# Kernel tuning notes

Measured on AMD Instinct MI355X. Metric: run time of the kernel, lower is better.

Reference implementation:

```python
import jax, jax.numpy as jnp
import numpy as np

NEG_SLOPE_GAT = 0.2   # PyG GATConv default negative_slope
NEG_SLOPE = 0.01      # torch.nn.LeakyReLU default
NUM_AISLES = 20       # aisle_nrs drawn from [0,20); matches aisle_nrs.max()+1


def leaky(x, s):
    return jnp.where(x >= 0, x, s * x)


def gat_conv(x, src, dst, W, a_src, a_dst, b, n_nodes):
    """Single-head PyG GATConv (self-loops already appended to src/dst)."""
    h = x @ W                                        # [N, C]
    es = h @ a_src                                   # [N]
    ed = h @ a_dst                                   # [N]
    e = leaky(es[src] + ed[dst], NEG_SLOPE_GAT)      # [E] per-edge score
    m = jax.ops.segment_max(e, dst, num_segments=n_nodes)
    w = jnp.exp(e - m[dst])
    z = jax.ops.segment_sum(w, dst, num_segments=n_nodes)
    alpha = w / z[dst]                               # segment softmax over incoming edges
    out = jax.ops.segment_sum(h[src] * alpha[:, None], dst, num_segments=n_nodes)
    return out + b


def setup_inputs() -> dict:
    key = jax.random.key(0)
    ks = jax.random.split(key, 32)
    B, N, E = 16, 2048, 32768
    Fin, H, O, HA = 32, 128, 64, 256

    def glorot(k, shape):
        fan = shape[0] + shape[-1]
        return jax.random.uniform(k, shape, jnp.float32, -1.0, 1.0) * np.sqrt(6.0 / fan)

    inp = {
        "graph_nodes": jax.random.normal(ks[0], (B, N, Fin), jnp.float32),
        "aisle_nrs": jax.random.randint(ks[1], (B, N), 0, NUM_AISLES),
        "graph_edge_links": jax.random.randint(ks[2], (B, 2, E), 0, N),
        "mask": jax.random.randint(ks[3], (B, N), 0, 2),
        "picks_left": jax.random.randint(ks[4], (B,), 0, 100),
        # GAT layer 1: Fin -> H
        "W1": glorot(ks[5], (Fin, H)), "as1": glorot(ks[6], (H,)), "ad1": glorot(ks[7], (H,)), "b1": jnp.zeros((H,), jnp.float32),
        # GAT layer 2: H -> H
        "W2": glorot(ks[8], (H, H)), "as2": glorot(ks[9], (H,)), "ad2": glorot(ks[10], (H,)), "b2": jnp.zeros((H,), jnp.float32),
        # GAT layer 3: H -> O
        "W3": glorot(ks[11], (H, O)), "as3": glorot(ks[12], (O,)), "ad3": glorot(ks[13], (O,)), "b3": jnp.zeros((O,), jnp.float32),
        # post-embedding MLP head
        "lw1": glorot(ks[14], (2 * O, HA)), "lb1": jnp.zeros((HA,), jnp.float32),
        "lw2": glorot(ks[15], (HA, O)), "lb2": jnp.zeros((O,), jnp.float32),
        "lw3": glorot(ks[16], (O, 1)), "lb3": jnp.zeros((1,), jnp.float32),
    }
    return inp


def reference(graph_nodes, aisle_nrs, graph_edge_links, mask, picks_left,
              W1, as1, ad1, b1, W2, as2, ad2, b2, W3, as3, ad3, b3,
              lw1, lb1, lw2, lb2, lw3, lb3):
    B, N, Fin = graph_nodes.shape
    NT = B * N
    x = graph_nodes.reshape(NT, Fin)

    # batch the graphs: offset per-graph edge indices, append self-loops
    off = (jnp.arange(B) * N)[:, None]
    src = (graph_edge_links[:, 0, :] + off).reshape(-1)
    dst = (graph_edge_links[:, 1, :] + off).reshape(-1)
    loops = jnp.arange(NT)
    src = jnp.concatenate([src, loops])
    dst = jnp.concatenate([dst, loops])

    x = gat_conv(x, src, dst, W1, as1, ad1, b1, NT)
    x = gat_conv(x, src, dst, W2, as2, ad2, b2, NT)
    x = gat_conv(x, src, dst, W3, as3, ad3, b3, NT)

    # scatter-mean aisle embedding
    batch_idx = jnp.repeat(jnp.arange(B), N)
    aid = aisle_nrs.reshape(-1) + batch_idx * NUM_AISLES   # [NT]
    S = B * NUM_AISLES
    ssum = jax.ops.segment_sum(x, aid, num_segments=S)
    cnt = jax.ops.segment_sum(jnp.ones((NT,), x.dtype), aid, num_segments=S)
    emb = ssum / jnp.maximum(cnt, 1.0)[:, None]

    x = jnp.concatenate([x, emb[aid]], axis=1)             # [NT, 2*O]
    x = leaky(x @ lw1 + lb1, NEG_SLOPE)
    x = leaky(x @ lw2 + lb2, NEG_SLOPE)
    x = (x @ lw3 + lb3).reshape(B, N)

    logits = jnp.where(mask != 0, x, -jnp.inf)
    return jax.nn.softmax(logits, axis=1)
```

## Files before the change

kernel.cpp:

```cpp
#include <hip/hip_runtime.h>
#include <hip/hip_bf16.h>
#include <math.h>
#include <stdint.h>

#define BATCH 16
#define NNODE 2048
#define EPG   32768
#define NT    (BATCH * NNODE)
#define ET    (BATCH * EPG + NT)
#define NUM_AISLES 20
#define SEG   (BATCH * NUM_AISLES)
#define NEG_GAT 0.2f
#define NEG_MLP 0.01f
#define ACHUNK 8
#define CAP 64
#define EMB_LD 72

typedef __attribute__((ext_vector_type(8))) short s16x8;
typedef __attribute__((ext_vector_type(4))) float f32x4;

__device__ __forceinline__ void split_bf16(float v, unsigned short& hi, unsigned short& lo) {
    unsigned int u = __float_as_uint(v);
    unsigned int r = u + 0x7FFFu + ((u >> 16) & 1u);
    hi = (unsigned short)(r >> 16);
    float fh = __uint_as_float(((unsigned int)hi) << 16);
    float rem = v - fh;
    unsigned int u2 = __float_as_uint(rem);
    unsigned int r2 = u2 + 0x7FFFu + ((u2 >> 16) & 1u);
    lo = (unsigned short)(r2 >> 16);
}

__device__ __forceinline__ unsigned int pack_bf16(float v) {
    unsigned short h, l;
    split_bf16(v, h, l);
    return ((unsigned int)h << 16) | l;
}

__device__ __forceinline__ float unpack_f32(unsigned int u) {
    return __uint_as_float(u & 0xffff0000u) + __uint_as_float(u << 16);
}

union SU { s16x8 v; unsigned short u[8]; };

__device__ __forceinline__ void unpack_pair(const uint4& u0, const uint4& u1, SU& ah, SU& al) {
    unsigned int uu[8] = {u0.x, u0.y, u0.z, u0.w, u1.x, u1.y, u1.z, u1.w};
#pragma unroll
    for (int j = 0; j < 8; ++j) {
        ah.u[j] = (unsigned short)(uu[j] >> 16);
        al.u[j] = (unsigned short)uu[j];
    }
}

__device__ __forceinline__ void split_pair(const float4& v0, const float4& v1, SU& ah, SU& al) {
    float a8[8] = {v0.x, v0.y, v0.z, v0.w, v1.x, v1.y, v1.z, v1.w};
#pragma unroll
    for (int j = 0; j < 8; ++j) split_bf16(a8[j], ah.u[j], al.u[j]);
}

__device__ __forceinline__ int swz_row0(int bx) {
    int xcd = bx & 7, i = bx >> 3;
    int graph = xcd * 2 + (i >> 5);
    return graph * NNODE + (i & 31) * 64;
}

template <int K, int KC, int NOUT, int COLS>
__device__ __forceinline__ void prep_one(const float* __restrict__ W,
                                         unsigned short* __restrict__ dst, int idx) {
    constexpr int SWM = (KC >= 64) ? 7 : 3;
    int k = idx / NOUT, col = idx - k * NOUT;
    int ch = k / KC, kl = k - ch * KC;
    int ct = col / COLS, n = col - ct * COLS;
    int tile = ct * (K / KC) + ch;
    unsigned short h, l;
    split_bf16(W[idx], h, l);
    size_t base = (size_t)tile * (2 * COLS * KC);
    int pos = n * KC + (kl ^ ((n & SWM) << 3));
    dst[base + pos] = h;
    dst[base + COLS * KC + pos] = l;
}

__global__ __launch_bounds__(256) void prep_weights(const float* __restrict__ W1,
                                                    const float* __restrict__ W2,
                                                    const float* __restrict__ W3,
                                                    const float* __restrict__ lw1,
                                                    const float* __restrict__ lw2,
                                                    unsigned short* __restrict__ P1,
                                                    unsigned short* __restrict__ P2,
                                                    unsigned short* __restrict__ P3,
                                                    unsigned short* __restrict__ P4,
                                                    unsigned short* __restrict__ P5,
                                                    int* __restrict__ cnt,
                                                    int* __restrict__ scount) {
    int b = blockIdx.x, t = threadIdx.x;
    if (b < 16)        prep_one<32, 32, 128, 128>(W1, P1, b * 256 + t);
    else if (b < 80)   prep_one<128, 64, 128, 128>(W2, P2, (b - 16) * 256 + t);
    else if (b < 112)  prep_one<128, 128, 64, 64>(W3, P3, (b - 80) * 256 + t);
    else if (b < 240)  prep_one<128, 64, 256, 128>(lw1, P4, (b - 112) * 256 + t);
    else if (b < 304)  prep_one<256, 128, 64, 64>(lw2, P5, (b - 240) * 256 + t);
    else if (b < 432)  cnt[(b - 304) * 256 + t] = 0;
    else if (t < BATCH) scount[t] = 0;
}

__device__ __forceinline__ void scatter_body(int b, const int* __restrict__ links,
                                             int* __restrict__ cnt,
                                             int* __restrict__ col_bkt) {
    int s, d;
    if (b < 2048) {
        int xcd = b & 7, idx = b >> 3;
        int g = xcd * 2 + (idx >> 7);
        int chunk = idx & 127;
        int i = chunk * 256 + threadIdx.x;
        const int* pb = links + (size_t)g * 2 * EPG;
        s = pb[i] + (g << 11);
        d = pb[EPG + i] + (g << 11);
    } else {
        int b2 = b - 2048;
        int xcd = b2 & 7, idx = b2 >> 3;
        int g = xcd * 2 + (idx >> 3);
        int chunk = idx & 7;
        s = d = g * NNODE + chunk * 256 + threadIdx.x;
    }
    int pos = atomicAdd(&cnt[d], 1);
    if (pos < CAP) col_bkt[d * CAP + pos] = s;
}

template <int K, int KC, int NOUT, int COLS, bool LEAKY, bool ATTN, bool FINAL,
          bool CONCAT, bool PACKEDA, bool PACKOUT>
__device__ __forceinline__ void gemm_body(int bx, int by,
                                          const void* __restrict__ Aptr,
                                          const unsigned short* __restrict__ WP,
                                          const float* __restrict__ bias,
                                          void* __restrict__ outp,
                                          const float* __restrict__ a_src,
                                          const float* __restrict__ a_dst,
                                          float* __restrict__ es,
                                          float* __restrict__ ed,
                                          const float* __restrict__ psum,
                                          const int* __restrict__ pcnt,
                                          const int* __restrict__ aisle,
                                          const float* __restrict__ lw3,
                                          const float* __restrict__ lb3,
                                          const int* __restrict__ mask,
                                          float* __restrict__ logits,
                                          int* __restrict__ scount,
                                          float* __restrict__ smout) {
    constexpr int C = COLS / 16;
    constexpr int SWM = (KC >= 64) ? 7 : 3;
    constexpr int TILE_US = COLS * KC;
    constexpr int TB2 = 2 * TILE_US * 2;
    constexpr int NCH = K / KC;
    constexpr int NKS = KC / 32;
    constexpr int NPRE = CONCAT ? 2 : (K / 32);
    static_assert(TB2 % 4096 == 0, "chunk must be a multiple of one 256-thread 16B sweep");

    __shared__ unsigned short WS[2 * TILE_US];
    __shared__ float emb_s[CONCAT ? NUM_AISLES * EMB_LD : 1];

    const int tid = threadIdx.x;
    const int wave = tid >> 6, lane = tid & 63;
    const int quad = lane >> 4, l15 = lane & 15;
    const int row0 = swz_row0(bx);
    const int m = row0 + wave * 16 + l15;

    uint4 apu[(CONCAT || PACKEDA) ? NPRE : 1][2];
    float4 apf[(CONCAT || PACKEDA) ? 1 : NPRE][2];
#pragma unroll
    for (int t = 0; t < NPRE; ++t) {
        const int off = t * 32 + quad * 8;
        if constexpr (CONCAT) {
            const unsigned int* ap = (const unsigned int*)Aptr + (size_t)m * 64 + off;
            apu[t][0] = ((const uint4*)ap)[0];
            apu[t][1] = ((const uint4*)ap)[1];
        } else if constexpr (PACKEDA) {
            const unsigned int* ap = (const unsigned int*)Aptr + (size_t)m * K + off;
            apu[t][0] = ((const uint4*)ap)[0];
            apu[t][1] = ((const uint4*)ap)[1];
        } else {
            const float* sp = (const float*)Aptr + (size_t)m * K + off;
            apf[t][0] = ((const float4*)sp)[0];
            apf[t][1] = ((const float4*)sp)[1];
        }
    }

    int am = 0;
    if constexpr (CONCAT) {
        int g = row0 >> 11;
        for (int i = tid; i < NUM_AISLES * 64; i += 256) {
            int a = i >> 6, f = i & 63;
            float s = 0.f;
            int c = 0;
#pragma unroll
            for (int ch = 0; ch < ACHUNK; ++ch) {
                s += psum[((size_t)(g * ACHUNK + ch) * NUM_AISLES + a) * 64 + f];
                c += pcnt[(g * ACHUNK + ch) * NUM_AISLES + a];
            }
            emb_s[a * EMB_LD + f] = s / fmaxf((float)c, 1.0f);
        }
        am = aisle[m];
    }

    f32x4 acc[C];
#pragma unroll
    for (int c = 0; c < C; ++c)
#pragma unroll
        for (int v = 0; v < 4; ++v) acc[c][v] = 0.f;

#pragma unroll
    for (int cidx = 0; cidx < NCH; ++cidx) {
        const char* gsrc = (const char*)WP + (size_t)(by * NCH + cidx) * TB2;
#pragma unroll
        for (int s = 0; s < TB2 / 4096; ++s) {
            __builtin_amdgcn_global_load_lds(
                (const __attribute__((address_space(1))) void*)(gsrc + s * 4096 + wave * 1024 + lane * 16),
                (__attribute__((address_space(3))) void*)&WS[(s * 4096 + wave * 1024) >> 1],
                16, 0, 0);
        }
        __syncthreads();

#pragma unroll
        for (int ks = 0; ks < NKS; ++ks) {
            const int t = cidx * NKS + ks;
            SU ah, al;
            if constexpr (CONCAT) {
                if (t < 2) {
                    unpack_pair(apu[t & 1][0], apu[t & 1][1], ah, al);
                } else {
                    const float* ep = &emb_s[am * EMB_LD + (t * 32 + quad * 8 - 64)];
                    split_pair(((const float4*)ep)[0], ((const float4*)ep)[1], ah, al);
                }
            } else if constexpr (PACKEDA) {
                unpack_pair(apu[t][0], apu[t][1], ah, al);
            } else {
                split_pair(apf[t][0], apf[t][1], ah, al);
            }

            const int kq = ks * 32 + quad * 8;
#pragma unroll
            for (int c = 0; c < C; ++c) {
                int n = c * 16 + l15;
                int pos = n * KC + (kq ^ ((n & SWM) << 3));
                s16x8 wh = *(const s16x8*)&WS[pos];
                s16x8 wl = *(const s16x8*)&WS[TILE_US + pos];
                acc[c] = __builtin_amdgcn_mfma_f32_16x16x32_bf16(ah.v, wh, acc[c], 0, 0, 0);
                acc[c] = __builtin_amdgcn_mfma_f32_16x16x32_bf16(ah.v, wl, acc[c], 0, 0, 0);
                acc[c] = __builtin_amdgcn_mfma_f32_16x16x32_bf16(al.v, wh, acc[c], 0, 0, 0);
            }
        }
        if (cidx + 1 < NCH) __syncthreads();
    }
    if constexpr (FINAL) {
        const int g = row0 >> 11;
#pragma unroll
        for (int reg = 0; reg < 4; ++reg) {
            float p = 0.f;
#pragma unroll
            for (int c = 0; c < C; ++c) {
                int colx = c * 16 + l15;
                float v = acc[c][reg] + bias[colx];
                v = v >= 0.f ? v : NEG_MLP * v;
                p += v * lw3[colx];
            }
#pragma unroll
            for (int mk = 1; mk < 16; mk <<= 1) p += __shfl_xor(p, mk, 64);
            if (l15 == 0) {
                int row = row0 + wave * 16 + quad * 4 + reg;
                float lg = p + lb3[0];
                logits[row] = (mask[row] != 0) ? lg : -INFINITY;
            }
        }
        __threadfence();
        __syncthreads();
        __shared__ int slast;
        if (tid == 0) slast = (atomicAdd(&scount[g], 1) == 31) ? 1 : 0;
        __syncthreads();
        if (slast) {
            __threadfence();
            const float* lr = logits + g * NNODE;
            float* op = smout + g * NNODE;
            __shared__ float sred[4], sredz[4];
            float mx = -INFINITY;
            for (int i = tid; i < NNODE; i += 256) mx = fmaxf(mx, lr[i]);
#pragma unroll
            for (int off = 32; off; off >>= 1) mx = fmaxf(mx, __shfl_xor(mx, off, 64));
            if (lane == 0) sred[wave] = mx;
            __syncthreads();
            mx = fmaxf(fmaxf(sred[0], sred[1]), fmaxf(sred[2], sred[3]));
            float z = 0.f;
            for (int i = tid; i < NNODE; i += 256) z += __expf(lr[i] - mx);
#pragma unroll
            for (int off = 32; off; off >>= 1) z += __shfl_xor(z, off, 64);
            if (lane == 0) sredz[wave] = z;
            __syncthreads();
            z = sredz[0] + sredz[1] + sredz[2] + sredz[3];
            float invz = 1.0f / z;
            for (int i = tid; i < NNODE; i += 256) {
                float v = lr[i];
                op[i] = (v == -INFINITY) ? 0.f : __expf(v - mx) * invz;
            }
        }
    } else {
#pragma unroll
        for (int c = 0; c < C; ++c) {
            int colx = by * COLS + c * 16 + l15;
            float bv = bias ? bias[colx] : 0.f;
#pragma unroll
            for (int reg = 0; reg < 4; ++reg) {
                int row = row0 + wave * 16 + quad * 4 + reg;
                float v = acc[c][reg] + bv;
                if (LEAKY) v = v >= 0.f ? v : NEG_MLP * v;
                if constexpr (PACKOUT) {
                    ((unsigned int*)outp)[(size_t)row * NOUT + colx] = pack_bf16(v);
                } else {
                    ((float*)outp)[(size_t)row * NOUT + colx] = v;
                }
            }
        }
        if constexpr (ATTN) {
#pragma unroll
            for (int reg = 0; reg < 4; ++reg) {
                float ps = 0.f, pd = 0.f;
#pragma unroll
                for (int c = 0; c < C; ++c) {
                    int colx = c * 16 + l15;
                    float v = acc[c][reg];
                    ps += v * a_src[colx];
                    pd += v * a_dst[colx];
                }
#pragma unroll
                for (int mk = 1; mk < 16; mk <<= 1) {
                    ps += __shfl_xor(ps, mk, 64);
                    pd += __shfl_xor(pd, mk, 64);
                }
                if (l15 == 0) {
                    int row = row0 + wave * 16 + quad * 4 + reg;
                    es[row] = ps;
                    ed[row] = pd;
                }
            }
        }
    }
}

template <int K, int KC, int NOUT, int COLS, bool LEAKY, bool ATTN, bool FINAL,
          bool CONCAT, bool PACKEDA, bool PACKOUT>
__global__ __launch_bounds__(256) void gemm_mfma(const void* __restrict__ A,
                                                 const unsigned short* __restrict__ WP,
                                                 const float* __restrict__ bias,
                                                 void* __restrict__ out,
                                                 const float* __restrict__ a_src,
                                                 const float* __restrict__ a_dst,
                                                 float* __restrict__ es,
                                                 float* __restrict__ ed,
                                                 const float* __restrict__ psum,
                                                 const int* __restrict__ pcnt,
                                                 const int* __restrict__ aisle,
                                                 const float* __restrict__ lw3,
                                                 const float* __restrict__ lb3,
                                                 const int* __restrict__ mask,
                                                 float* __restrict__ logits,
                                                 int* __restrict__ scount,
                                                 float* __restrict__ smout) {
    gemm_body<K, KC, NOUT, COLS, LEAKY, ATTN, FINAL, CONCAT, PACKEDA, PACKOUT>(
        blockIdx.x, blockIdx.y, A, WP, bias, out, a_src, a_dst, es, ed,
        psum, pcnt, aisle, lw3, lb3, mask, logits, scount, smout);
}

__global__ __launch_bounds__(256) void gemm1_scatter(const float* __restrict__ A,
                                                     const unsigned short* __restrict__ WP,
                                                     float* __restrict__ out,
                                                     const float* __restrict__ a_src,
                                                     const float* __restrict__ a_dst,
                                                     float* __restrict__ es,
                                                     float* __restrict__ ed,
                                                     const int* __restrict__ links,
                                                     int* __restrict__ cnt,
                                                     int* __restrict__ col_bkt) {
    if (blockIdx.x >= NT / 64) {
        scatter_body(blockIdx.x - NT / 64, links, cnt, col_bkt);
        return;
    }
    gemm_body<32, 32, 128, 128, false, true, false, false, false, false>(
        blockIdx.x, 0, A, WP, nullptr, out, a_src, a_dst, es, ed,
        nullptr, nullptr, nullptr, nullptr, nullptr, nullptr, nullptr, nullptr, nullptr);
}

template <int HD>
__global__ __launch_bounds__(256) void gat_aggregate(const float* __restrict__ h,
                                                     const float* __restrict__ es,
                                                     const float* __restrict__ ed,
                                                     const int* __restrict__ cnt,
                                                     const int* __restrict__ col_bkt,
                                                     const float* __restrict__ bias,
                                                     unsigned int* __restrict__ out) {
    int b = blockIdx.x;
    int xcd = b & 7, q = b >> 3;
    int graph = xcd * 2 + (q >> 9);
    int node = graph * NNODE + (q & 511) * 4 + (threadIdx.x >> 6);
    int lane = threadIdx.x & 63;
    int deg = cnt[node];
    deg = deg < CAP ? deg : CAP;
    float edv = ed[node];

    float e0 = -INFINITY;
    int c0v = 0;
    if (lane < deg) {
        c0v = col_bkt[node * CAP + lane];
        float e = es[c0v] + edv;
        e0 = e >= 0.f ? e : NEG_GAT * e;
    }
    float m = e0;
#pragma unroll
    for (int off = 32; off; off >>= 1) m = fmaxf(m, __shfl_xor(m, off, 64));
    float z = __expf(e0 - m);
#pragma unroll
    for (int off = 32; off; off >>= 1) z += __shfl_xor(z, off, 64);
    float w0 = __expf(e0 - m) / z;

    const int quad = lane >> 4, l15 = lane & 15;
    if (HD == 128) {
        float a0 = 0.f, a1 = 0.f, a2 = 0.f, a3 = 0.f;
        float a4 = 0.f, a5 = 0.f, a6 = 0.f, a7 = 0.f;
        for (int jj = 0; jj < deg; jj += 4) {
            int j2 = jj + quad;
            int s = __shfl(c0v, j2, 64);
            float w = __shfl(w0, j2, 64);
            const float* base = h + (size_t)s * 128 + l15 * 8;
            float4 v0 = *(const float4*)base;
            float4 v1 = *(const float4*)(base + 4);
            a0 += w * v0.x; a1 += w * v0.y; a2 += w * v0.z; a3 += w * v0.w;
            a4 += w * v1.x; a5 += w * v1.y; a6 += w * v1.z; a7 += w * v1.w;
        }
#pragma unroll
        for (int off = 16; off <= 32; off <<= 1) {
            a0 += __shfl_xor(a0, off, 64); a1 += __shfl_xor(a1, off, 64);
            a2 += __shfl_xor(a2, off, 64); a3 += __shfl_xor(a3, off, 64);
            a4 += __shfl_xor(a4, off, 64); a5 += __shfl_xor(a5, off, 64);
            a6 += __shfl_xor(a6, off, 64); a7 += __shfl_xor(a7, off, 64);
        }
        if (quad == 0) {
            const float* bb = bias + l15 * 8;
            uint4 p0, p1;
            p0.x = pack_bf16(a0 + bb[0]); p0.y = pack_bf16(a1 + bb[1]);
            p0.z = pack_bf16(a2 + bb[2]); p0.w = pack_bf16(a3 + bb[3]);
            p1.x = pack_bf16(a4 + bb[4]); p1.y = pack_bf16(a5 + bb[5]);
            p1.z = pack_bf16(a6 + bb[6]); p1.w = pack_bf16(a7 + bb[7]);
            unsigned int* op = out + (size_t)node * 128 + l15 * 8;
            *(uint4*)op = p0;
            *(uint4*)(op + 4) = p1;
        }
    } else {
        float a0 = 0.f, a1 = 0.f, a2 = 0.f, a3 = 0.f;
        for (int jj = 0; jj < deg; jj += 4) {
            int j2 = jj + quad;
            int s = __shfl(c0v, j2, 64);
            float w = __shfl(w0, j2, 64);
            float4 v = *(const float4*)(h + (size_t)s * 64 + l15 * 4);
            a0 += w * v.x; a1 += w * v.y; a2 += w * v.z; a3 += w * v.w;
        }
#pragma unroll
        for (int off = 16; off <= 32; off <<= 1) {
            a0 += __shfl_xor(a0, off, 64); a1 += __shfl_xor(a1, off, 64);
            a2 += __shfl_xor(a2, off, 64); a3 += __shfl_xor(a3, off, 64);
        }
        if (quad == 0) {
            const float* bb = bias + l15 * 4;
            uint4 p;
            p.x = pack_bf16(a0 + bb[0]); p.y = pack_bf16(a1 + bb[1]);
            p.z = pack_bf16(a2 + bb[2]); p.w = pack_bf16(a3 + bb[3]);
            *(uint4*)(out + (size_t)node * 64 + l15 * 4) = p;
        }
    }
}

__global__ __launch_bounds__(256) void aisle_partial(const unsigned int* __restrict__ x3,
                                                     const int* __restrict__ aisle,
                                                     float* __restrict__ psum,
                                                     int* __restrict__ pcnt) {
    int xcd = blockIdx.x & 7, idx = blockIdx.x >> 3;
    int g = xcd * 2 + (idx >> 3);
    int ch = idx & 7;
    int pb = g * ACHUNK + ch;
    int f = threadIdx.x & 63;
    int stripe = threadIdx.x >> 6;

    __shared__ float sacc[4][NUM_AISLES][64];
    __shared__ int scnt[4][NUM_AISLES];
    for (int i = threadIdx.x; i < 4 * NUM_AISLES * 64; i += 256)
        ((float*)sacc)[i] = 0.f;
    for (int i = threadIdx.x; i < 4 * NUM_AISLES; i += 256)
        ((int*)scnt)[i] = 0;
    __syncthreads();

    const int* ai = aisle + g * NNODE;
    const unsigned int* xg = x3 + (size_t)g * NNODE * 64;
    int n0 = ch * 256 + stripe * 64;
#pragma unroll 4
    for (int i = 0; i < 64; ++i) {
        int n = n0 + i;
        int a = ai[n];
        float v = unpack_f32(xg[(size_t)n * 64 + f]);
        sacc[stripe][a][f] += v;
        if (f == 0) scnt[stripe][a]++;
    }
    __syncthreads();

    for (int i = threadIdx.x; i < NUM_AISLES * 64; i += 256) {
        int a = i >> 6, ff = i & 63;
        psum[((size_t)pb * NUM_AISLES + a) * 64 + ff] =
            sacc[0][a][ff] + sacc[1][a][ff] + sacc[2][a][ff] + sacc[3][a][ff];
    }
    for (int i = threadIdx.x; i < NUM_AISLES; i += 256) {
        pcnt[pb * NUM_AISLES + i] =
            scnt[0][i] + scnt[1][i] + scnt[2][i] + scnt[3][i];
    }
}


extern "C" void kernel_launch(void* const* d_in, const int* in_sizes, int n_in,
                              void* d_out, int out_size, void* d_ws, size_t ws_size,
                              hipStream_t stream) {
    const float* gn   = (const float*)d_in[0];
    const int* aisle  = (const int*)d_in[1];
    const int* links  = (const int*)d_in[2];
    const int* mask   = (const int*)d_in[3];
    const float* W1  = (const float*)d_in[5];
    const float* as1 = (const float*)d_in[6];
    const float* ad1 = (const float*)d_in[7];
    const float* b1  = (const float*)d_in[8];
    const float* W2  = (const float*)d_in[9];
    const float* as2 = (const float*)d_in[10];
    const float* ad2 = (const float*)d_in[11];
    const float* b2  = (const float*)d_in[12];
    const float* W3  = (const float*)d_in[13];
    const float* as3 = (const float*)d_in[14];
    const float* ad3 = (const float*)d_in[15];
    const float* b3  = (const float*)d_in[16];
    const float* lw1 = (const float*)d_in[17];
    const float* lb1 = (const float*)d_in[18];
    const float* lw2 = (const float*)d_in[19];
    const float* lb2 = (const float*)d_in[20];
    const float* lw3 = (const float*)d_in[21];
    const float* lb3 = (const float*)d_in[22];
    float* out = (float*)d_out;

    float* ws = (float*)d_ws;
    float* h      = ws;
    float* xb     = h + (size_t)NT * 128;
    float* es     = xb + (size_t)NT * 128;
    float* ed     = es + NT;
    float* emb    = ed + NT;
    float* y1     = emb + SEG * 64;
    float* y2     = y1 + (size_t)NT * 256;
    float* logits = y2 + (size_t)NT * 64;
    float* psum   = logits + NT;
    int* pcnt     = (int*)(psum + 128 * NUM_AISLES * 64);
    int* row_ptr  = pcnt + 128 * NUM_AISLES;
    int* cnt      = row_ptr + NT + 1;
    int* scount   = cnt + NT;
    int* col_bkt  = (int*)y2;

    unsigned short* wsplit = (unsigned short*)(((uintptr_t)(scount + BATCH) + 255) & ~(uintptr_t)255);
    unsigned short* P1 = wsplit;
    unsigned short* P2 = P1 + 8192;
    unsigned short* P3 = P2 + 32768;
    unsigned short* P4 = P3 + 16384;
    unsigned short* P5 = P4 + 65536;

    const int EB = (ET + 255) / 256;

    prep_weights<<<433, 256, 0, stream>>>(W1, W2, W3, lw1, lw2, P1, P2, P3, P4, P5, cnt, scount);

    gemm1_scatter<<<NT / 64 + EB, 256, 0, stream>>>(gn, P1, h, as1, ad1, es, ed,
                                                    links, cnt, col_bkt);
    gat_aggregate<128><<<NT / 4, 256, 0, stream>>>(h, es, ed, cnt, col_bkt, b1, (unsigned int*)xb);

    gemm_mfma<128, 64, 128, 128, false, true, false, false, true, false><<<dim3(NT / 64, 1), 256, 0, stream>>>(
        xb, P2, nullptr, h, as2, ad2, es, ed, nullptr, nullptr, nullptr, nullptr, nullptr, nullptr, nullptr, nullptr, nullptr);
    gat_aggregate<128><<<NT / 4, 256, 0, stream>>>(h, es, ed, cnt, col_bkt, b2, (unsigned int*)xb);

    gemm_mfma<128, 128, 64, 64, false, true, false, false, true, false><<<dim3(NT / 64, 1), 256, 0, stream>>>(
        xb, P3, nullptr, h, as3, ad3, es, ed, nullptr, nullptr, nullptr, nullptr, nullptr, nullptr, nullptr, nullptr, nullptr);
    gat_aggregate<64><<<NT / 4, 256, 0, stream>>>(h, es, ed, cnt, col_bkt, b3, (unsigned int*)xb);

    aisle_partial<<<BATCH * ACHUNK, 256, 0, stream>>>((const unsigned int*)xb, aisle, psum, pcnt);

    gemm_mfma<128, 64, 256, 128, true, false, false, true, false, true><<<dim3(NT / 64, 2), 256, 0, stream>>>(
        xb, P4, lb1, y1, nullptr, nullptr, nullptr, nullptr, psum, pcnt, aisle, nullptr, nullptr, nullptr, nullptr, nullptr, nullptr);

    gemm_mfma<256, 128, 64, 64, true, false, true, false, true, false><<<dim3(NT / 64, 1), 256, 0, stream>>>(
        y1, P5, lb2, nullptr, nullptr, nullptr, nullptr, nullptr, nullptr, nullptr, nullptr, lw3, lb3, mask, logits, scount, out);
}
```

Baseline: 313.1 us.

## Split GEMM block columns across wave pairs, halving rows per block

Each 256-thread GEMM block now covers 32 rows instead of 64. The four waves form a 2x2 grid: two row groups times two column halves, so each wave computes half the output columns. Partial dot products for the attention scores and the final logit are combined through a small shared array with an extra barrier. Launching twice as many blocks is meant to raise occupancy and parallelism across CUs. The cost is twice the weight-tile loads into LDS per row and an additional __syncthreads.

Result: slower. 371.3 us (+18.6%).

```diff
diff --git a/kernel.cpp b/kernel.cpp
--- a/kernel.cpp
+++ b/kernel.cpp
@@ -59,8 +59,8 @@
 
 __device__ __forceinline__ int swz_row0(int bx) {
     int xcd = bx & 7, i = bx >> 3;
-    int graph = xcd * 2 + (i >> 5);
-    return graph * NNODE + (i & 31) * 64;
+    int graph = xcd * 2 + (i >> 6);
+    return graph * NNODE + (i & 63) * 32;
 }
 
 template <int K, int KC, int NOUT, int COLS>
@@ -144,7 +144,7 @@
                                           float* __restrict__ logits,
                                           int* __restrict__ scount,
                                           float* __restrict__ smout) {
-    constexpr int C = COLS / 16;
+    constexpr int C = COLS / 32;
     constexpr int SWM = (KC >= 64) ? 7 : 3;
     constexpr int TILE_US = COLS * KC;
     constexpr int TB2 = 2 * TILE_US * 2;
@@ -155,12 +155,16 @@
 
     __shared__ unsigned short WS[2 * TILE_US];
     __shared__ float emb_s[CONCAT ? NUM_AISLES * EMB_LD : 1];
+    __shared__ float2 comb[(ATTN || FINAL) ? 32 : 1];
 
     const int tid = threadIdx.x;
     const int wave = tid >> 6, lane = tid & 63;
     const int quad = lane >> 4, l15 = lane & 15;
+    const int rw = wave & 1;
+    const int chf = wave >> 1;
+    const int cb = chf * (COLS / 2);
     const int row0 = swz_row0(bx);
-    const int m = row0 + wave * 16 + l15;
+    const int m = row0 + rw * 16 + l15;
 
     uint4 apu[(CONCAT || PACKEDA) ? NPRE : 1][2];
     float4 apf[(CONCAT || PACKEDA) ? 1 : NPRE][2];
@@ -237,7 +241,7 @@
             const int kq = ks * 32 + quad * 8;
 #pragma unroll
             for (int c = 0; c < C; ++c) {
-                int n = c * 16 + l15;
+                int n = cb + c * 16 + l15;
                 int pos = n * KC + (kq ^ ((n & SWM) << 3));
                 s16x8 wh = *(const s16x8*)&WS[pos];
                 s16x8 wl = *(const s16x8*)&WS[TILE_US + pos];
@@ -250,28 +254,40 @@
     }
     if constexpr (FINAL) {
         const int g = row0 >> 11;
+        float pr[4];
 #pragma unroll
         for (int reg = 0; reg < 4; ++reg) {
             float p = 0.f;
 #pragma unroll
             for (int c = 0; c < C; ++c) {
-                int colx = c * 16 + l15;
+                int colx = cb + c * 16 + l15;
                 float v = acc[c][reg] + bias[colx];
                 v = v >= 0.f ? v : NEG_MLP * v;
                 p += v * lw3[colx];
             }
 #pragma unroll
             for (int mk = 1; mk < 16; mk <<= 1) p += __shfl_xor(p, mk, 64);
-            if (l15 == 0) {
-                int row = row0 + wave * 16 + quad * 4 + reg;
-                float lg = p + lb3[0];
+            pr[reg] = p;
+        }
+        if (chf == 1 && l15 == 0) {
+#pragma unroll
+            for (int reg = 0; reg < 4; ++reg)
+                comb[rw * 16 + quad * 4 + reg].x = pr[reg];
+        }
+        __syncthreads();
+        if (chf == 0 && l15 == 0) {
+#pragma unroll
+            for (int reg = 0; reg < 4; ++reg) {
+                int lr = rw * 16 + quad * 4 + reg;
+                int row = row0 + lr;
+                float lg = pr[reg] + comb[lr].x + lb3[0];
                 logits[row] = (mask[row] != 0) ? lg : -INFINITY;
             }
         }
         __threadfence();
         __syncthreads();
         __shared__ int slast;
-        if (tid == 0) slast = (atomicAdd(&scount[g], 1) == 31) ? 1 : 0;
+        if (tid == 0) slast = (atomicAdd(&scount[g], 1) == 63) ? 1 : 0;
         __syncthreads();
         if (slast) {
             __threadfence();
@@ -301,11 +317,11 @@
     } else {
 #pragma unroll
         for (int c = 0; c < C; ++c) {
-            int colx = by * COLS + c * 16 + l15;
+            int colx = by * COLS + cb + c * 16 + l15;
             float bv = bias ? bias[colx] : 0.f;
 #pragma unroll
             for (int reg = 0; reg < 4; ++reg) {
-                int row = row0 + wave * 16 + quad * 4 + reg;
+                int row = row0 + rw * 16 + quad * 4 + reg;
                 float v = acc[c][reg] + bv;
                 if (LEAKY) v = v >= 0.f ? v : NEG_MLP * v;
                 if constexpr (PACKOUT) {
@@ -316,12 +332,13 @@
             }
         }
         if constexpr (ATTN) {
+            float psr[4], pdr[4];
 #pragma unroll
             for (int reg = 0; reg < 4; ++reg) {
                 float ps = 0.f, pd = 0.f;
 #pragma unroll
                 for (int c = 0; c < C; ++c) {
-                    int colx = c * 16 + l15;
+                    int colx = cb + c * 16 + l15;
                     float v = acc[c][reg];
                     ps += v * a_src[colx];
                     pd += v * a_dst[colx];
@@ -331,10 +348,24 @@
                     ps += __shfl_xor(ps, mk, 64);
                     pd += __shfl_xor(pd, mk, 64);
                 }
-                if (l15 == 0) {
-                    int row = row0 + wave * 16 + quad * 4 + reg;
-                    es[row] = ps;
-                    ed[row] = pd;
+                psr[reg] = ps;
+                pdr[reg] = pd;
+            }
+            if (chf == 1 && l15 == 0) {
+#pragma unroll
+                for (int reg = 0; reg < 4; ++reg) {
+                    comb[rw * 16 + quad * 4 + reg].x = psr[reg];
+                    comb[rw * 16 + quad * 4 + reg].y = pdr[reg];
+                }
+            }
+            __syncthreads();
+            if (chf == 0 && l15 == 0) {
+#pragma unroll
+                for (int reg = 0; reg < 4; ++reg) {
+                    int lr = rw * 16 + quad * 4 + reg;
+                    int row = row0 + lr;
+                    es[row] = psr[reg] + comb[lr].x;
+                    ed[row] = pdr[reg] + comb[lr].y;
                 }
             }
         }
@@ -375,8 +406,8 @@
                                                      const int* __restrict__ links,
                                                      int* __restrict__ cnt,
                                                      int* __restrict__ col_bkt) {
-    if (blockIdx.x >= NT / 64) {
-        scatter_body(blockIdx.x - NT / 64, links, cnt, col_bkt);
+    if (blockIdx.x >= NT / 32) {
+        scatter_body(blockIdx.x - NT / 32, links, cnt, col_bkt);
         return;
     }
     gemm_body<32, 32, 128, 128, false, true, false, false, false, false>(
@@ -570,23 +601,23 @@
 
     prep_weights<<<433, 256, 0, stream>>>(W1, W2, W3, lw1, lw2, P1, P2, P3, P4, P5, cnt, scount);
 
-    gemm1_scatter<<<NT / 64 + EB, 256, 0, stream>>>(gn, P1, h, as1, ad1, es, ed,
+    gemm1_scatter<<<NT / 32 + EB, 256, 0, stream>>>(gn, P1, h, as1, ad1, es, ed,
                                                     links, cnt, col_bkt);
     gat_aggregate<128><<<NT / 4, 256, 0, stream>>>(h, es, ed, cnt, col_bkt, b1, (unsigned int*)xb);
 
-    gemm_mfma<128, 64, 128, 128, false, true, false, false, true, false><<<dim3(NT / 64, 1), 256, 0, stream>>>(
+    gemm_mfma<128, 64, 128, 128, false, true, false, false, true, false><<<dim3(NT / 32, 1), 256, 0, stream>>>(
         xb, P2, nullptr, h, as2, ad2, es, ed, nullptr, nullptr, nullptr, nullptr, nullptr, nullptr, nullptr, nullptr, nullptr);
     gat_aggregate<128><<<NT / 4, 256, 0, stream>>>(h, es, ed, cnt, col_bkt, b2, (unsigned int*)xb);
 
-    gemm_mfma<128, 128, 64, 64, false, true, false, false, true, false><<<dim3(NT / 64, 1), 256, 0, stream>>>(
+    gemm_mfma<128, 128, 64, 64, false, true, false, false, true, false><<<dim3(NT / 32, 1), 256, 0, stream>>>(
         xb, P3, nullptr, h, as3, ad3, es, ed, nullptr, nullptr, nullptr, nullptr, nullptr, nullptr, nullptr, nullptr, nullptr);
     gat_aggregate<64><<<NT / 4, 256, 0, stream>>>(h, es, ed, cnt, col_bkt, b3, (unsigned int*)xb);
 
     aisle_partial<<<BATCH * ACHUNK, 256, 0, stream>>>((const unsigned int*)xb, aisle, psum, pcnt);
 
-    gemm_mfma<128, 64, 256, 128, true, false, false, true, false, true><<<dim3(NT / 64, 2), 256, 0, stream>>>(
+    gemm_mfma<128, 64, 256, 128, true, false, false, true, false, true><<<dim3(NT / 32, 2), 256, 0, stream>>>(
         xb, P4, lb1, y1, nullptr, nullptr, nullptr, nullptr, psum, pcnt, aisle, nullptr, nullptr, nullptr, nullptr, nullptr, nullptr);
 
-    gemm_mfma<256, 128, 64, 64, true, false, true, false, true, false><<<dim3(NT / 64, 1), 256, 0, stream>>>(
+    gemm_mfma<256, 128, 64, 64, true, false, true, false, true, false><<<dim3(NT / 32, 1), 256, 0, stream>>>(
         y1, P5, lb2, nullptr, nullptr, nullptr, nullptr, nullptr, nullptr, nullptr, nullptr, lw3, lb3, mask, logits, scount, out);
 }
```

## Stage A operand tiles through LDS via async global_load_lds with XOR swizzle

Applied to the files above, without the earlier changes.

Replaces the per-lane register prefetch of all A-operand K-slices with chunked asynchronous global-to-LDS copies of a 64-row A tile, read back through an XOR-swizzled slot layout to avoid bank conflicts. The aim is to cut register pressure and get coalesced wide loads that arrive alongside the W chunk copies. In exchange it adds LDS usage, which may lower occupancy, and A data now waits on the same barrier as W instead of being prefetched up front.

Result: no change. 313.2 us (+0.0%).

```diff
diff --git a/kernel.cpp b/kernel.cpp
--- a/kernel.cpp
+++ b/kernel.cpp
@@ -150,37 +150,23 @@
     constexpr int TB2 = 2 * TILE_US * 2;
     constexpr int NCH = K / KC;
     constexpr int NKS = KC / 32;
-    constexpr int NPRE = CONCAT ? 2 : (K / 32);
-    static_assert(TB2 % 4096 == 0, "chunk must be a multiple of one 256-thread 16B sweep");
+    constexpr int ABYTES = 64 * KC * 4;
+    constexpr int SPR = KC / 4;
+    constexpr int AROWB = CONCAT ? 256 : K * 4;
+    static_assert(TB2 % 4096 == 0, "W chunk must be a multiple of one 256-thread 16B sweep");
+    static_assert(ABYTES % 4096 == 0, "A chunk must be a multiple of one 256-thread 16B sweep");
+    static_assert(SPR >= 8, "A slot-swizzle needs >=8 slots/row");
 
     __shared__ unsigned short WS[2 * TILE_US];
+    __shared__ unsigned int AS[64 * KC];
     __shared__ float emb_s[CONCAT ? NUM_AISLES * EMB_LD : 1];
 
     const int tid = threadIdx.x;
     const int wave = tid >> 6, lane = tid & 63;
     const int quad = lane >> 4, l15 = lane & 15;
     const int row0 = swz_row0(bx);
-    const int m = row0 + wave * 16 + l15;
-
-    uint4 apu[(CONCAT || PACKEDA) ? NPRE : 1][2];
-    float4 apf[(CONCAT || PACKEDA) ? 1 : NPRE][2];
-#pragma unroll
-    for (int t = 0; t < NPRE; ++t) {
-        const int off = t * 32 + quad * 8;
-        if constexpr (CONCAT) {
-            const unsigned int* ap = (const unsigned int*)Aptr + (size_t)m * 64 + off;
-            apu[t][0] = ((const uint4*)ap)[0];
-            apu[t][1] = ((const uint4*)ap)[1];
-        } else if constexpr (PACKEDA) {
-            const unsigned int* ap = (const unsigned int*)Aptr + (size_t)m * K + off;
-            apu[t][0] = ((const uint4*)ap)[0];
-            apu[t][1] = ((const uint4*)ap)[1];
-        } else {
-            const float* sp = (const float*)Aptr + (size_t)m * K + off;
-            apf[t][0] = ((const float4*)sp)[0];
-            apf[t][1] = ((const float4*)sp)[1];
-        }
-    }
+    const int arow = wave * 16 + l15;
+    const int m = row0 + arow;
 
     int am = 0;
     if constexpr (CONCAT) {
@@ -215,6 +201,21 @@
                 (__attribute__((address_space(3))) void*)&WS[(s * 4096 + wave * 1024) >> 1],
                 16, 0, 0);
         }
+        if (!CONCAT || cidx == 0) {
+#pragma unroll
+            for (int s = 0; s < ABYTES / 4096; ++s) {
+                int idx16 = s * 256 + tid;
+                int row_l = idx16 / SPR;
+                int slot = idx16 - row_l * SPR;
+                int ssrc = slot ^ (row_l & 7);
+                const char* asrc = (const char*)Aptr + (size_t)(row0 + row_l) * AROWB
+                                 + (size_t)cidx * KC * 4 + ssrc * 16;
+                __builtin_amdgcn_global_load_lds(
+                    (const __attribute__((address_space(1))) void*)asrc,
+                    (__attribute__((address_space(3))) void*)((char*)AS + (size_t)idx16 * 16),
+                    16, 0, 0);
+            }
+        }
         __syncthreads();
 
 #pragma unroll
@@ -223,15 +224,27 @@
             SU ah, al;
             if constexpr (CONCAT) {
                 if (t < 2) {
-                    unpack_pair(apu[t & 1][0], apu[t & 1][1], ah, al);
+                    const char* ab = (const char*)AS + arow * (KC * 4);
+                    int slot0 = ks * 8 + quad * 2;
+                    uint4 au0 = *(const uint4*)(ab + ((slot0 ^ (arow & 7)) * 16));
+                    uint4 au1 = *(const uint4*)(ab + (((slot0 + 1) ^ (arow & 7)) * 16));
+                    unpack_pair(au0, au1, ah, al);
                 } else {
                     const float* ep = &emb_s[am * EMB_LD + (t * 32 + quad * 8 - 64)];
                     split_pair(((const float4*)ep)[0], ((const float4*)ep)[1], ah, al);
                 }
             } else if constexpr (PACKEDA) {
-                unpack_pair(apu[t][0], apu[t][1], ah, al);
+                const char* ab = (const char*)AS + arow * (KC * 4);
+                int slot0 = ks * 8 + quad * 2;
+                uint4 au0 = *(const uint4*)(ab + ((slot0 ^ (arow & 7)) * 16));
+                uint4 au1 = *(const uint4*)(ab + (((slot0 + 1) ^ (arow & 7)) * 16));
+                unpack_pair(au0, au1, ah, al);
             } else {
-                split_pair(apf[t][0], apf[t][1], ah, al);
+                const char* ab = (const char*)AS + arow * (KC * 4);
+                int slot0 = ks * 8 + quad * 2;
+                float4 f0 = *(const float4*)(ab + ((slot0 ^ (arow & 7)) * 16));
+                float4 f1 = *(const float4*)(ab + (((slot0 + 1) ^ (arow & 7)) * 16));
+                split_pair(f0, f1, ah, al);
             }
 
             const int kq = ks * 32 + quad * 8;
```
